# Kernel tuning notes

Hardware: AMD Instinct MI355X
Metric: run time of the kernel (lower is better)

## Reference

```python
import jax, jax.numpy as jnp
import numpy as np

HIDDEN = 2048
N_HEADS = 32
N_KV_HEADS = 8
HEAD_DIM = HIDDEN // N_HEADS  # 64
N_REP = N_HEADS // N_KV_HEADS  # 4
ROPE_THETA = 10000.0


def setup_inputs() -> dict:
    key = jax.random.key(0)
    ks = jax.random.split(key, 5)
    b, s = 2, 2048
    x = jax.random.normal(ks[0], (b, s, HIDDEN), dtype=jnp.float32)
    position_ids = jnp.arange(b * s, dtype=jnp.int32).reshape(b, s)
    sc = 1.0 / np.sqrt(HIDDEN)
    Wq = jax.random.normal(ks[1], (HIDDEN, HIDDEN), dtype=jnp.float32) * sc
    Wk = jax.random.normal(ks[2], (HIDDEN, N_KV_HEADS * HEAD_DIM), dtype=jnp.float32) * sc
    Wv = jax.random.normal(ks[3], (HIDDEN, N_KV_HEADS * HEAD_DIM), dtype=jnp.float32) * sc
    Wo = jax.random.normal(ks[4], (HIDDEN, HIDDEN), dtype=jnp.float32) * sc
    return {"input_ids": x, "Wq": Wq, "Wk": Wk, "Wv": Wv, "Wo": Wo,
            "position_ids": position_ids}


def _rope_cos_sin(position_ids, dtype):
    # inv_freq: [head_dim/2]
    inv_freq = 1.0 / (ROPE_THETA ** (jnp.arange(0, HEAD_DIM, 2, dtype=jnp.float32) / HEAD_DIM))
    freqs = position_ids.astype(jnp.float32)[..., None] * inv_freq  # [b, s, d/2]
    emb = jnp.concatenate([freqs, freqs], axis=-1)  # [b, s, d]
    return emb.astype(dtype), None  # placeholder, replaced below


def _rotate_half(x):
    x1, x2 = jnp.split(x, 2, axis=-1)
    return jnp.concatenate([-x2, x1], axis=-1)


def reference(input_ids, Wq, Wk, Wv, Wo, position_ids):
    b, s, _ = input_ids.shape
    q = (input_ids @ Wq).reshape(b, s, N_HEADS, HEAD_DIM).transpose(0, 2, 1, 3)      # [b,H,s,d]
    k = (input_ids @ Wk).reshape(b, s, N_KV_HEADS, HEAD_DIM).transpose(0, 2, 1, 3)   # [b,Hkv,s,d]
    v = (input_ids @ Wv).reshape(b, s, N_KV_HEADS, HEAD_DIM).transpose(0, 2, 1, 3)

    # RoPE
    inv_freq = 1.0 / (ROPE_THETA ** (jnp.arange(0, HEAD_DIM, 2, dtype=jnp.float32) / HEAD_DIM))
    freqs = position_ids.astype(jnp.float32)[..., None] * inv_freq  # [b,s,d/2]
    emb = jnp.concatenate([freqs, freqs], axis=-1)                   # [b,s,d]
    cos = jnp.cos(emb).astype(input_ids.dtype)[:, None, :, :]        # [b,1,s,d]
    sin = jnp.sin(emb).astype(input_ids.dtype)[:, None, :, :]
    q = q * cos + _rotate_half(q) * sin
    k = k * cos + _rotate_half(k) * sin

    # repeat_kv: [b,Hkv,s,d] -> [b,H,s,d]
    k = jnp.repeat(k, N_REP, axis=1)
    v = jnp.repeat(v, N_REP, axis=1)

    # causal SDPA
    scale = 1.0 / np.sqrt(HEAD_DIM)
    scores = jnp.einsum('bhqd,bhkd->bhqk', q, k) * scale
    causal = jnp.tril(jnp.ones((s, s), dtype=bool))
    scores = jnp.where(causal, scores, jnp.finfo(scores.dtype).min)
    attn = jax.nn.softmax(scores, axis=-1)
    out = jnp.einsum('bhqk,bhkd->bhqd', attn, v)                     # [b,H,s,d]
    out = out.transpose(0, 2, 1, 3).reshape(b, s, HIDDEN)
    return out @ Wo
```

## Files before the change

kernel.cpp:

```cpp
#include <hip/hip_runtime.h>
#include <hip/hip_bf16.h>

#define HIDDEN 2048
#define NHEADS 32
#define NKVH   8
#define HD     64
#define BATCH  2
#define SEQ    2048
#define ROWS   (BATCH * SEQ)
#define NQKV   3072
#define KCOL   2048
#define VCOL   2560

typedef __bf16 bf16x8 __attribute__((ext_vector_type(8)));
typedef __bf16 bf16x4 __attribute__((ext_vector_type(4)));
typedef float  f32x4  __attribute__((ext_vector_type(4)));
typedef short  s16x4  __attribute__((ext_vector_type(4)));
typedef short  s16x8  __attribute__((ext_vector_type(8)));

__device__ __forceinline__ void gl2lds16(const void* g, void* l) {
  __builtin_amdgcn_global_load_lds(
      (const __attribute__((address_space(1))) void*)g,
      (__attribute__((address_space(3))) void*)l, 16, 0, 0);
}

__device__ __forceinline__ short f2bs(float f) {
  __bf16 h = (__bf16)f;
  return __builtin_bit_cast(short, h);
}

__device__ __forceinline__ float fexp2(float x) {
#if __has_builtin(__builtin_amdgcn_exp2f)
  return __builtin_amdgcn_exp2f(x);
#else
  return exp2f(x);
#endif
}

__device__ __forceinline__ f32x4 mfma16(s16x4 a, s16x4 b, f32x4 c) {
#if __has_builtin(__builtin_amdgcn_mfma_f32_16x16x16bf16_1k)
  return __builtin_amdgcn_mfma_f32_16x16x16bf16_1k(a, b, c, 0, 0, 0);
#else
  s16x8 a8 = __builtin_shufflevector(a, (s16x4){0,0,0,0}, 0,1,2,3,4,5,6,7);
  s16x8 b8 = __builtin_shufflevector(b, (s16x4){0,0,0,0}, 0,1,2,3,4,5,6,7);
  a8[4]=0;a8[5]=0;a8[6]=0;a8[7]=0; b8[4]=0;b8[5]=0;b8[6]=0;b8[7]=0;
  return __builtin_amdgcn_mfma_f32_16x16x32_bf16(
      __builtin_bit_cast(bf16x8, a8), __builtin_bit_cast(bf16x8, b8), c, 0, 0, 0);
#endif
}

__global__ void prep(const float* __restrict__ Wq, const float* __restrict__ Wk,
                     const float* __restrict__ Wv, const float* __restrict__ Wo,
                     const float* __restrict__ x,
                     __bf16* __restrict__ dstW, __bf16* __restrict__ Xb) {
  __shared__ __bf16 tile[32][33];
  int bid = blockIdx.x, tid = threadIdx.x;
  if (bid < 10240) {
    int n0 = (bid % 160) * 32, k0 = (bid / 160) * 32;
    int tx = tid & 31, ty = tid >> 5;
    const float* src;
    int N, c0;
    if (n0 < 2048)      { src = Wq; N = 2048; c0 = n0; }
    else if (n0 < 2560) { src = Wk; N = 512;  c0 = n0 - 2048; }
    else if (n0 < 3072) { src = Wv; N = 512;  c0 = n0 - 2560; }
    else                { src = Wo; N = 2048; c0 = n0 - 3072; }
#pragma unroll
    for (int i = 0; i < 32; i += 8)
      tile[ty + i][tx] = (__bf16)src[(size_t)(k0 + ty + i) * N + (c0 + tx)];
    __syncthreads();
#pragma unroll
    for (int i = 0; i < 32; i += 8)
      dstW[(size_t)(n0 + ty + i) * HIDDEN + (k0 + tx)] = tile[tx][ty + i];
  } else {
    size_t i = (size_t)(bid - 10240) * 256 + tid;
    const float4* s = (const float4*)(x + i * 16);
    float4 a = s[0], b = s[1], c = s[2], d = s[3];
    bf16x8 o0, o1;
    o0[0] = (__bf16)a.x; o0[1] = (__bf16)a.y; o0[2] = (__bf16)a.z; o0[3] = (__bf16)a.w;
    o0[4] = (__bf16)b.x; o0[5] = (__bf16)b.y; o0[6] = (__bf16)b.z; o0[7] = (__bf16)b.w;
    o1[0] = (__bf16)c.x; o1[1] = (__bf16)c.y; o1[2] = (__bf16)c.z; o1[3] = (__bf16)c.w;
    o1[4] = (__bf16)d.x; o1[5] = (__bf16)d.y; o1[6] = (__bf16)d.z; o1[7] = (__bf16)d.w;
    *(bf16x8*)(Xb + i * 16)     = o0;
    *(bf16x8*)(Xb + i * 16 + 8) = o1;
  }
}

template <typename OutT, bool ROPE>
__launch_bounds__(256, 2)
__global__ void gemm_bt(const __bf16* __restrict__ A, const __bf16* __restrict__ Bt,
                        OutT* __restrict__ C, int M, int N, int K,
                        const int* __restrict__ pos_ids, __bf16* __restrict__ Vt) {
  __shared__ __bf16 As[2][128 * 32];
  __shared__ __bf16 Bs[2][128 * 32];
  int id = blockIdx.x;
  int bm = (id & 7) * 4 + ((id >> 3) & 3);
  int bn = id >> 5;
  int t = threadIdx.x;
  int wave = t >> 6, lane = t & 63, l16 = lane & 15, quad = lane >> 4;
  int wm = (wave >> 1) * 64, wn = (wave & 1) * 64;

  f32x4 acc[4][4] = {};

  int arow = t >> 2;
  int ac   = (t & 3) * 8;
  const __bf16* Ag = A  + (size_t)(bm * 128 + arow) * K + ac;
  const __bf16* Bg = Bt + (size_t)(bn * 128 + arow) * K + ac;
  int woff = wave * 512;

  for (int k0 = 0; k0 < K; k0 += 64) {
    __syncthreads();
    gl2lds16(Ag + k0,                      &As[0][woff]);
    gl2lds16(Ag + (size_t)64 * K + k0,      &As[0][2048 + woff]);
    gl2lds16(Ag + k0 + 32,                 &As[1][woff]);
    gl2lds16(Ag + (size_t)64 * K + k0 + 32, &As[1][2048 + woff]);
    gl2lds16(Bg + k0,                      &Bs[0][woff]);
    gl2lds16(Bg + (size_t)64 * K + k0,      &Bs[0][2048 + woff]);
    gl2lds16(Bg + k0 + 32,                 &Bs[1][woff]);
    gl2lds16(Bg + (size_t)64 * K + k0 + 32, &Bs[1][2048 + woff]);
    __syncthreads();

#pragma unroll
    for (int ks = 0; ks < 2; ++ks) {
      bf16x8 af[4], bfr[4];
#pragma unroll
      for (int i = 0; i < 4; ++i) {
        af[i]  = *(const bf16x8*)(&As[ks][(wm + i * 16 + l16) * 32 + quad * 8]);
        bfr[i] = *(const bf16x8*)(&Bs[ks][(wn + i * 16 + l16) * 32 + quad * 8]);
      }
#pragma unroll
      for (int i = 0; i < 4; ++i)
#pragma unroll
        for (int j = 0; j < 4; ++j)
          acc[i][j] = __builtin_amdgcn_mfma_f32_16x16x32_bf16(af[i], bfr[j], acc[i][j], 0, 0, 0);
    }
  }

  if (ROPE) {
    int headidx = bn * 2 + (wn >> 6);
    if (headidx >= 40) {
#pragma unroll
      for (int i = 0; i < 4; ++i) {
        int srow = bm * 128 + wm + i * 16 + quad * 4;
        int b = srow >> 11, s = srow & 2047;
#pragma unroll
        for (int j = 0; j < 4; ++j) {
          int vcol = bn * 128 + wn + j * 16 + l16 - VCOL;
          int hk = vcol >> 6, d = vcol & 63;
          bf16x4 w;
#pragma unroll
          for (int r = 0; r < 4; ++r) w[r] = (__bf16)acc[i][j][r];
          *(bf16x4*)(Vt + ((size_t)(b * NKVH + hk) * HD + d) * SEQ + s) = w;
        }
      }
      return;
    }
    float invrev0 = __expf(-(float)l16 * 0.28782313662425574f) * 0.15915494309189535f;
    float invrev1 = __expf(-(float)(l16 + 16) * 0.28782313662425574f) * 0.15915494309189535f;
#pragma unroll
    for (int i = 0; i < 4; ++i)
#pragma unroll
      for (int r = 0; r < 4; ++r) {
        int gr = bm * 128 + wm + i * 16 + quad * 4 + r;
        float pos = (float)pos_ids[gr];
        float rv0 = pos * invrev0; rv0 -= floorf(rv0);
        float rv1 = pos * invrev1; rv1 -= floorf(rv1);
        float a0 = rv0 * 6.283185307179586f, a1 = rv1 * 6.283185307179586f;
        float s0 = __sinf(a0), c0 = __cosf(a0);
        float s1 = __sinf(a1), c1 = __cosf(a1);
        float x0 = acc[i][0][r], x2 = acc[i][2][r];
        acc[i][0][r] = x0 * c0 - x2 * s0;
        acc[i][2][r] = x2 * c0 + x0 * s0;
        float x1 = acc[i][1][r], x3 = acc[i][3][r];
        acc[i][1][r] = x1 * c1 - x3 * s1;
        acc[i][3][r] = x3 * c1 + x1 * s1;
      }
  }

#pragma unroll
  for (int i = 0; i < 4; ++i)
#pragma unroll
    for (int j = 0; j < 4; ++j)
#pragma unroll
      for (int r = 0; r < 4; ++r)
        C[(size_t)(bm * 128 + wm + i * 16 + quad * 4 + r) * N +
          (bn * 128 + wn + j * 16 + l16)] = (OutT)acc[i][j][r];
}

__launch_bounds__(256, 4)
__global__ void flash_attn(const __bf16* __restrict__ QKV, const __bf16* __restrict__ Vt,
                           __bf16* __restrict__ O) {
  int wgid = blockIdx.x + 64 * (blockIdx.y + 8 * (int)blockIdx.z);
  int xcd  = wgid & 7;
  int j    = wgid >> 3;
  int G    = j >> 6;
  int gid  = xcd * 2 + G;
  int b    = gid >> 3;
  int hk   = gid & 7;
  int r    = j & 63;
  int b0   = r & 1, b5 = (r >> 5) & 1;
  int h    = hk * 4 + b0 + 2 * b5;
  int M0   = (r >> 1) & 15;
  int M    = (b0 ^ b5) ? (15 - M0) : M0;
  int NT   = 2 * M + 2;

  int t = threadIdx.x;
  int wave = t >> 6, lane = t & 63, l16 = lane & 15, quad = lane >> 4;

  __shared__ __bf16 Ks[2][2][64 * 32];
  __shared__ __bf16 Vs[2][4096];

  const __bf16* Kbase = QKV + (size_t)(b * SEQ) * NQKV + KCOL + hk * HD;
  const __bf16* VtB   = Vt + (size_t)(b * NKVH + hk) * HD * SEQ;

  int kr = wave * 16 + (lane >> 2);
  int kc = (lane & 3) * 8;
  int vd = kr;
  int vsc = (lane & 3) * 16;
  int vs4w = (lane & 3) * 4;

  const s16x4 vones = { (short)0x3F80, (short)0x3F80, (short)0x3F80, (short)0x3F80 };

  bf16x8 qfrag[2][2];
#pragma unroll
  for (int qi = 0; qi < 2; ++qi) {
    const __bf16* qp = QKV + (size_t)(b * SEQ + M * 128 + qi * 64 + wave * 16 + l16) * NQKV
                     + h * HD + quad * 8;
    bf16x8 q0 = *(const bf16x8*)qp;
    bf16x8 q1 = *(const bf16x8*)(qp + 32);
#pragma unroll
    for (int e = 0; e < 8; ++e) {
      qfrag[qi][0][e] = (__bf16)((float)q0[e] * 0.18033688011112042f);
      qfrag[qi][1][e] = (__bf16)((float)q1[e] * 0.18033688011112042f);
    }
  }

  f32x4 lacc[2] = { {0.f,0.f,0.f,0.f}, {0.f,0.f,0.f,0.f} };
  f32x4 oacc[2][4];
#pragma unroll
  for (int qi = 0; qi < 2; ++qi)
#pragma unroll
    for (int dt = 0; dt < 4; ++dt) oacc[qi][dt] = (f32x4){0.f, 0.f, 0.f, 0.f};

  {
    const __bf16* kp = Kbase + (size_t)kr * NQKV + kc;
    gl2lds16(kp,      &Ks[0][0][wave * 512]);
    gl2lds16(kp + 32, &Ks[0][1][wave * 512]);
    const __bf16* vp = VtB + (size_t)vd * SEQ + vsc;
    s16x8 v0 = __builtin_bit_cast(s16x8, *(const bf16x8*)vp);
    s16x8 v1 = __builtin_bit_cast(s16x8, *(const bf16x8*)(vp + 8));
    *(s16x4*)(&Vs[0][(vs4w + 0) * 256 + vd * 4]) = __builtin_shufflevector(v0, v0, 0, 1, 2, 3);
    *(s16x4*)(&Vs[0][(vs4w + 1) * 256 + vd * 4]) = __builtin_shufflevector(v0, v0, 4, 5, 6, 7);
    *(s16x4*)(&Vs[0][(vs4w + 2) * 256 + vd * 4]) = __builtin_shufflevector(v1, v1, 0, 1, 2, 3);
    *(s16x4*)(&Vs[0][(vs4w + 3) * 256 + vd * 4]) = __builtin_shufflevector(v1, v1, 4, 5, 6, 7);
  }

  for (int kt = 0; kt < NT; ++kt) {
    int buf = kt & 1;
    __syncthreads();

    bool pre = (kt < NT - 1);
    s16x8 pv0, pv1;
    if (pre) {
      const __bf16* kp = Kbase + (size_t)((kt + 1) * 64 + kr) * NQKV + kc;
      gl2lds16(kp,      &Ks[buf ^ 1][0][wave * 512]);
      gl2lds16(kp + 32, &Ks[buf ^ 1][1][wave * 512]);
      const __bf16* vp = VtB + (size_t)vd * SEQ + (kt + 1) * 64 + vsc;
      pv0 = __builtin_bit_cast(s16x8, *(const bf16x8*)vp);
      pv1 = __builtin_bit_cast(s16x8, *(const bf16x8*)(vp + 8));
    }

    f32x4 s0[4], s1[4];
#pragma unroll
    for (int nt = 0; nt < 4; ++nt) {
      s0[nt] = (f32x4){0.f, 0.f, 0.f, 0.f};
      s1[nt] = (f32x4){0.f, 0.f, 0.f, 0.f};
    }
#pragma unroll
    for (int ks = 0; ks < 2; ++ks) {
      bf16x8 kf[4];
#pragma unroll
      for (int nt = 0; nt < 4; ++nt)
        kf[nt] = *(const bf16x8*)(&Ks[buf][ks][(nt * 16 + l16) * 32 + quad * 8]);
#pragma unroll
      for (int nt = 0; nt < 4; ++nt)
        s1[nt] = __builtin_amdgcn_mfma_f32_16x16x32_bf16(kf[nt], qfrag[1][ks], s1[nt], 0, 0, 0);
      if (pre) {
#pragma unroll
        for (int nt = 0; nt < 4; ++nt)
          s0[nt] = __builtin_amdgcn_mfma_f32_16x16x32_bf16(kf[nt], qfrag[0][ks], s0[nt], 0, 0, 0);
      }
    }

    s16x4 af0[4], af1[4];
    {
      int qg = wave * 16 + l16;
      if (kt == NT - 1) {
#pragma unroll
        for (int nt = 0; nt < 4; ++nt)
#pragma unroll
          for (int rr = 0; rr < 4; ++rr) {
            int kg = nt * 16 + quad * 4 + rr;
            af1[nt][rr] = f2bs(fexp2((kg > qg) ? -1e30f : s1[nt][rr]));
          }
      } else {
#pragma unroll
        for (int nt = 0; nt < 4; ++nt)
#pragma unroll
          for (int rr = 0; rr < 4; ++rr)
            af1[nt][rr] = f2bs(fexp2(s1[nt][rr]));
      }
      if (pre) {
        if (kt == NT - 2) {
#pragma unroll
          for (int nt = 0; nt < 4; ++nt)
#pragma unroll
            for (int rr = 0; rr < 4; ++rr) {
              int kg = nt * 16 + quad * 4 + rr;
              af0[nt][rr] = f2bs(fexp2((kg > qg) ? -1e30f : s0[nt][rr]));
            }
        } else {
#pragma unroll
          for (int nt = 0; nt < 4; ++nt)
#pragma unroll
            for (int rr = 0; rr < 4; ++rr)
              af0[nt][rr] = f2bs(fexp2(s0[nt][rr]));
        }
      }
    }

#pragma unroll
    for (int nt = 0; nt < 4; ++nt) {
      s16x4 vf[4];
#pragma unroll
      for (int dt = 0; dt < 4; ++dt)
        vf[dt] = *(const s16x4*)(&Vs[buf][(nt * 4 + quad) * 256 + (dt * 16 + l16) * 4]);
#pragma unroll
      for (int dt = 0; dt < 4; ++dt)
        oacc[1][dt] = mfma16(af1[nt], vf[dt], oacc[1][dt]);
      lacc[1] = mfma16(af1[nt], vones, lacc[1]);
      if (pre) {
#pragma unroll
        for (int dt = 0; dt < 4; ++dt)
          oacc[0][dt] = mfma16(af0[nt], vf[dt], oacc[0][dt]);
        lacc[0] = mfma16(af0[nt], vones, lacc[0]);
      }
    }

    if (pre) {
      *(s16x4*)(&Vs[buf ^ 1][(vs4w + 0) * 256 + vd * 4]) = __builtin_shufflevector(pv0, pv0, 0, 1, 2, 3);
      *(s16x4*)(&Vs[buf ^ 1][(vs4w + 1) * 256 + vd * 4]) = __builtin_shufflevector(pv0, pv0, 4, 5, 6, 7);
      *(s16x4*)(&Vs[buf ^ 1][(vs4w + 2) * 256 + vd * 4]) = __builtin_shufflevector(pv1, pv1, 0, 1, 2, 3);
      *(s16x4*)(&Vs[buf ^ 1][(vs4w + 3) * 256 + vd * 4]) = __builtin_shufflevector(pv1, pv1, 4, 5, 6, 7);
    }
  }

#pragma unroll
  for (int qi = 0; qi < 2; ++qi) {
#pragma unroll
    for (int rr = 0; rr < 4; ++rr) {
      float inv = 1.0f / lacc[qi][rr];
#pragma unroll
      for (int dt = 0; dt < 4; ++dt) {
        float o = oacc[qi][dt][rr] * inv;
        O[(size_t)(b * SEQ + M * 128 + qi * 64 + wave * 16 + quad * 4 + rr) * HIDDEN +
          h * HD + dt * 16 + l16] = (__bf16)o;
      }
    }
  }
}

extern "C" void kernel_launch(void* const* d_in, const int* in_sizes, int n_in,
                              void* d_out, int out_size, void* d_ws, size_t ws_size,
                              hipStream_t stream) {
  const float* x  = (const float*)d_in[0];
  const float* Wq = (const float*)d_in[1];
  const float* Wk = (const float*)d_in[2];
  const float* Wv = (const float*)d_in[3];
  const float* Wo = (const float*)d_in[4];
  const int* pos  = (const int*)d_in[5];

  __bf16* Wqkvt = (__bf16*)d_ws;
  __bf16* Wot   = Wqkvt + (size_t)NQKV * HIDDEN;
  __bf16* Xb    = Wot + (size_t)HIDDEN * HIDDEN;
  __bf16* QKV   = Xb + (size_t)ROWS * HIDDEN;
  __bf16* Oat   = QKV + (size_t)ROWS * NQKV;
  __bf16* Vt    = Xb;

  prep<<<dim3(12288), 256, 0, stream>>>(Wq, Wk, Wv, Wo, x, Wqkvt, Xb);

  gemm_bt<__bf16, true><<<dim3(768), 256, 0, stream>>>(
      Xb, Wqkvt, QKV, ROWS, NQKV, HIDDEN, pos, Vt);

  flash_attn<<<dim3(64, NKVH, BATCH), 256, 0, stream>>>(QKV, Vt, Oat);

  gemm_bt<float, false><<<dim3(512), 256, 0, stream>>>(
      Oat, Wot, (float*)d_out, ROWS, HIDDEN, HIDDEN, nullptr, nullptr);
}
```

Before: 273.8 us.

## Vectorize weight transpose prep, swizzle K LDS reads, load V directly from global

The weight transpose/convert kernel now processes 32x128 tiles with float4 loads and 16-byte bf16 stores, cutting the block count from 10240 to 2560. In flash attention, the K tile is loaded with an XOR-swizzled column offset to avoid LDS bank conflicts. The V LDS staging buffer is removed: V fragments are read straight from global (L2-resident Vt) each iteration, with no prefetch into LDS. This drops LDS writes and their shuffles, but exposes global load latency inside the loop and adds register pressure.

```diff
diff --git a/kernel.cpp b/kernel.cpp
--- a/kernel.cpp
+++ b/kernel.cpp
@@ -53,26 +53,41 @@
                      const float* __restrict__ Wv, const float* __restrict__ Wo,
                      const float* __restrict__ x,
                      __bf16* __restrict__ dstW, __bf16* __restrict__ Xb) {
-  __shared__ __bf16 tile[32][33];
-  int bid = blockIdx.x, tid = threadIdx.x;
-  if (bid < 10240) {
-    int n0 = (bid % 160) * 32, k0 = (bid / 160) * 32;
-    int tx = tid & 31, ty = tid >> 5;
+  int bid = blockIdx.x, t = threadIdx.x;
+  if (bid < 2560) {
+    __shared__ __bf16 tl[32][132];
+    int k0 = (bid & 15) * 128;
+    int n0 = (bid >> 4) * 32;
     const float* src;
     int N, c0;
     if (n0 < 2048)      { src = Wq; N = 2048; c0 = n0; }
     else if (n0 < 2560) { src = Wk; N = 512;  c0 = n0 - 2048; }
     else if (n0 < 3072) { src = Wv; N = 512;  c0 = n0 - 2560; }
     else                { src = Wo; N = 2048; c0 = n0 - 3072; }
-#pragma unroll
-    for (int i = 0; i < 32; i += 8)
-      tile[ty + i][tx] = (__bf16)src[(size_t)(k0 + ty + i) * N + (c0 + tx)];
+    int rr = t >> 3;
+    int cc = (t & 7) * 4;
+#pragma unroll
+    for (int pass = 0; pass < 4; ++pass) {
+      int k = pass * 32 + rr;
+      float4 v = *(const float4*)(src + (size_t)(k0 + k) * N + c0 + cc);
+      tl[cc + 0][k] = (__bf16)v.x;
+      tl[cc + 1][k] = (__bf16)v.y;
+      tl[cc + 2][k] = (__bf16)v.z;
+      tl[cc + 3][k] = (__bf16)v.w;
+    }
     __syncthreads();
-#pragma unroll
-    for (int i = 0; i < 32; i += 8)
-      dstW[(size_t)(n0 + ty + i) * HIDDEN + (k0 + tx)] = tile[tx][ty + i];
+    int n = t >> 4;
+    int ch = t & 15;
+#pragma unroll
+    for (int it = 0; it < 2; ++it) {
+      int nn = n + it * 16;
+      s16x4 lo = *(const s16x4*)(&tl[nn][ch * 8]);
+      s16x4 hi = *(const s16x4*)(&tl[nn][ch * 8 + 4]);
+      s16x8 o = __builtin_shufflevector(lo, hi, 0, 1, 2, 3, 4, 5, 6, 7);
+      *(s16x8*)(dstW + (size_t)(n0 + nn) * HIDDEN + k0 + ch * 8) = o;
+    }
   } else {
-    size_t i = (size_t)(bid - 10240) * 256 + tid;
+    size_t i = (size_t)(bid - 2560) * 256 + t;
     const float4* s = (const float4*)(x + i * 16);
     float4 a = s[0], b = s[1], c = s[2], d = s[3];
     bf16x8 o0, o1;
@@ -207,16 +222,15 @@
   int wave = t >> 6, lane = t & 63, l16 = lane & 15, quad = lane >> 4;
 
   __shared__ __bf16 Ks[2][2][64 * 32];
-  __shared__ __bf16 Vs[2][4096];
 
   const __bf16* Kbase = QKV + (size_t)(b * SEQ) * NQKV + KCOL + hk * HD;
   const __bf16* VtB   = Vt + (size_t)(b * NKVH + hk) * HD * SEQ;
 
-  int kr = wave * 16 + (lane >> 2);
-  int kc = (lane & 3) * 8;
-  int vd = kr;
-  int vsc = (lane & 3) * 16;
-  int vs4w = (lane & 3) * 4;
+  int kr  = wave * 16 + (lane >> 2);
+  int kcs = ((lane & 3) ^ ((lane >> 3) & 3)) * 8;
+  int rq  = (quad ^ ((l16 >> 1) & 3)) * 8;
+
+  const __bf16* vb0 = VtB + (size_t)l16 * SEQ + quad * 4;
 
   const s16x4 vones = { (short)0x3F80, (short)0x3F80, (short)0x3F80, (short)0x3F80 };
 
@@ -242,16 +256,9 @@
     for (int dt = 0; dt < 4; ++dt) oacc[qi][dt] = (f32x4){0.f, 0.f, 0.f, 0.f};
 
   {
-    const __bf16* kp = Kbase + (size_t)kr * NQKV + kc;
+    const __bf16* kp = Kbase + (size_t)kr * NQKV + kcs;
     gl2lds16(kp,      &Ks[0][0][wave * 512]);
     gl2lds16(kp + 32, &Ks[0][1][wave * 512]);
-    const __bf16* vp = VtB + (size_t)vd * SEQ + vsc;
-    s16x8 v0 = __builtin_bit_cast(s16x8, *(const bf16x8*)vp);
-    s16x8 v1 = __builtin_bit_cast(s16x8, *(const bf16x8*)(vp + 8));
-    *(s16x4*)(&Vs[0][(vs4w + 0) * 256 + vd * 4]) = __builtin_shufflevector(v0, v0, 0, 1, 2, 3);
-    *(s16x4*)(&Vs[0][(vs4w + 1) * 256 + vd * 4]) = __builtin_shufflevector(v0, v0, 4, 5, 6, 7);
-    *(s16x4*)(&Vs[0][(vs4w + 2) * 256 + vd * 4]) = __builtin_shufflevector(v1, v1, 0, 1, 2, 3);
-    *(s16x4*)(&Vs[0][(vs4w + 3) * 256 + vd * 4]) = __builtin_shufflevector(v1, v1, 4, 5, 6, 7);
   }
 
   for (int kt = 0; kt < NT; ++kt) {
@@ -259,14 +266,10 @@
     __syncthreads();
 
     bool pre = (kt < NT - 1);
-    s16x8 pv0, pv1;
     if (pre) {
-      const __bf16* kp = Kbase + (size_t)((kt + 1) * 64 + kr) * NQKV + kc;
+      const __bf16* kp = Kbase + (size_t)((kt + 1) * 64 + kr) * NQKV + kcs;
       gl2lds16(kp,      &Ks[buf ^ 1][0][wave * 512]);
       gl2lds16(kp + 32, &Ks[buf ^ 1][1][wave * 512]);
-      const __bf16* vp = VtB + (size_t)vd * SEQ + (kt + 1) * 64 + vsc;
-      pv0 = __builtin_bit_cast(s16x8, *(const bf16x8*)vp);
-      pv1 = __builtin_bit_cast(s16x8, *(const bf16x8*)(vp + 8));
     }
 
     f32x4 s0[4], s1[4];
@@ -280,7 +283,7 @@
       bf16x8 kf[4];
 #pragma unroll
       for (int nt = 0; nt < 4; ++nt)
-        kf[nt] = *(const bf16x8*)(&Ks[buf][ks][(nt * 16 + l16) * 32 + quad * 8]);
+        kf[nt] = *(const bf16x8*)(&Ks[buf][ks][(nt * 16 + l16) * 32 + rq]);
 #pragma unroll
       for (int nt = 0; nt < 4; ++nt)
         s1[nt] = __builtin_amdgcn_mfma_f32_16x16x32_bf16(kf[nt], qfrag[1][ks], s1[nt], 0, 0, 0);
@@ -289,6 +292,16 @@
         for (int nt = 0; nt < 4; ++nt)
           s0[nt] = __builtin_amdgcn_mfma_f32_16x16x32_bf16(kf[nt], qfrag[0][ks], s0[nt], 0, 0, 0);
       }
+    }
+
+    s16x4 vf[4][4];
+    {
+      const __bf16* vbk = vb0 + kt * 64;
+#pragma unroll
+      for (int dt = 0; dt < 4; ++dt)
+#pragma unroll
+        for (int nt = 0; nt < 4; ++nt)
+          vf[nt][dt] = *(const s16x4*)(vbk + (size_t)dt * 16 * SEQ + nt * 16);
     }
 
     s16x4 af0[4], af1[4];
@@ -330,27 +343,16 @@
 
 #pragma unroll
     for (int nt = 0; nt < 4; ++nt) {
-      s16x4 vf[4];
 #pragma unroll
       for (int dt = 0; dt < 4; ++dt)
-        vf[dt] = *(const s16x4*)(&Vs[buf][(nt * 4 + quad) * 256 + (dt * 16 + l16) * 4]);
-#pragma unroll
-      for (int dt = 0; dt < 4; ++dt)
-        oacc[1][dt] = mfma16(af1[nt], vf[dt], oacc[1][dt]);
+        oacc[1][dt] = mfma16(af1[nt], vf[nt][dt], oacc[1][dt]);
       lacc[1] = mfma16(af1[nt], vones, lacc[1]);
       if (pre) {
 #pragma unroll
         for (int dt = 0; dt < 4; ++dt)
-          oacc[0][dt] = mfma16(af0[nt], vf[dt], oacc[0][dt]);
+          oacc[0][dt] = mfma16(af0[nt], vf[nt][dt], oacc[0][dt]);
         lacc[0] = mfma16(af0[nt], vones, lacc[0]);
       }
-    }
-
-    if (pre) {
-      *(s16x4*)(&Vs[buf ^ 1][(vs4w + 0) * 256 + vd * 4]) = __builtin_shufflevector(pv0, pv0, 0, 1, 2, 3);
-      *(s16x4*)(&Vs[buf ^ 1][(vs4w + 1) * 256 + vd * 4]) = __builtin_shufflevector(pv0, pv0, 4, 5, 6, 7);
-      *(s16x4*)(&Vs[buf ^ 1][(vs4w + 2) * 256 + vd * 4]) = __builtin_shufflevector(pv1, pv1, 0, 1, 2, 3);
-      *(s16x4*)(&Vs[buf ^ 1][(vs4w + 3) * 256 + vd * 4]) = __builtin_shufflevector(pv1, pv1, 4, 5, 6, 7);
     }
   }
 
@@ -386,7 +388,7 @@
   __bf16* Oat   = QKV + (size_t)ROWS * NQKV;
   __bf16* Vt    = Xb;
 
-  prep<<<dim3(12288), 256, 0, stream>>>(Wq, Wk, Wv, Wo, x, Wqkvt, Xb);
+  prep<<<dim3(4608), 256, 0, stream>>>(Wq, Wk, Wv, Wo, x, Wqkvt, Xb);
 
   gemm_bt<__bf16, true><<<dim3(768), 256, 0, stream>>>(
       Xb, Wqkvt, QKV, ROWS, NQKV, HIDDEN, pos, Vt);
```

Measured after the change: 341.5 us. 24.7% more time.
